# Optimization experiments

Measured on AMD Instinct MI355X. Metric: run time of the kernel, lower is better.

Reference implementation:

```python
import jax, jax.numpy as jnp
import numpy as np


def _conv(x, w, b, pad):
    y = jax.lax.conv_general_dilated(x, w, (1, 1), pad,
                                     dimension_numbers=('NCHW', 'OIHW', 'NCHW'))
    return y + b[None, :, None, None]


def _prelu(x, a):
    return jnp.where(x >= 0, x, a[None, :, None, None] * x)


def _pool2(x):
    # adaptive_avg_pool2d to exactly half resolution == 2x2 mean pooling
    B, C, H, W = x.shape
    return x.reshape(B, C, H // 2, 2, W // 2, 2).mean(axis=(3, 5))


def _l2norm(v, axis=-1):
    return v / jnp.maximum(jnp.linalg.norm(v, axis=axis, keepdims=True), 1e-12)


def _caun(x_low, ctx, w1, b1, a1, w2, b2, a2, kw, kb, sf=2):
    B, C, H, W = x_low.shape
    if ctx.shape[-2:] != (H, W):
        ctx = _pool2(ctx)
    f = _prelu(_conv(ctx, w1, b1, 'SAME'), a1)
    f = _prelu(_conv(f, w2, b2, 'SAME'), a2)
    mask = _conv(f, kw, kb, 'VALID')  # 1x1 conv -> [B, C*9*sf*sf, H, W]
    m = jax.nn.softmax(mask.reshape(B, C, 9, sf, sf, H, W), axis=2)
    xp = jnp.pad(x_low, ((0, 0), (0, 0), (1, 1), (1, 1)), mode='edge')
    # 3x3 neighborhoods in F.unfold row-major order -> [B, C, 9, H, W]
    neigh = jnp.stack([xp[:, :, i:i + H, j:j + W]
                       for i in range(3) for j in range(3)], axis=2)
    out = jnp.einsum('bcnuvhw,bcnhw->bcuvhw', m, neigh)  # [B,C,sf,sf,H,W]
    # faithful to torch permute(0,1,5,3,4,2).reshape(B,C,H*sf,W*sf)
    out = jnp.transpose(out, (0, 1, 5, 3, 4, 2)).reshape(B, C, H * sf, W * sf)
    return out


def _block(x, w1, b1, w2, b2):
    x = jax.nn.relu(_conv(x, w1, b1, 'SAME'))
    return jax.nn.relu(_conv(x, w2, b2, 'SAME'))


def setup_inputs() -> dict:
    key = jax.random.key(0)
    ks = iter(jax.random.split(key, 64))
    def rnd(shape, s=0.05):
        return jax.random.normal(next(ks), shape, jnp.float32) * s
    d = {}
    # encoder features (B=2, base 256x256, channels [32,64,128,256])
    d['x0_0'] = rnd((2, 32, 256, 256), 1.0)
    d['x1_0'] = rnd((2, 64, 128, 128), 1.0)
    d['x2_0'] = rnd((2, 128, 64, 64), 1.0)
    d['x3_0'] = rnd((2, 256, 32, 32), 1.0)
    # caun3: in=256, ctx=128
    d['c3_w1'] = rnd((128, 128, 3, 3)); d['c3_b1'] = jnp.zeros(128)
    d['c3_a1'] = 0.25 * jnp.ones(128)
    d['c3_w2'] = rnd((64, 128, 3, 3)); d['c3_b2'] = jnp.zeros(64)
    d['c3_a2'] = 0.25 * jnp.ones(64)
    d['c3_kw'] = rnd((256 * 36, 64, 1, 1)); d['c3_kb'] = jnp.zeros(256 * 36)
    # caun2: in=128, ctx=64
    d['c2_w1'] = rnd((64, 64, 3, 3)); d['c2_b1'] = jnp.zeros(64)
    d['c2_a1'] = 0.25 * jnp.ones(64)
    d['c2_w2'] = rnd((32, 64, 3, 3)); d['c2_b2'] = jnp.zeros(32)
    d['c2_a2'] = 0.25 * jnp.ones(32)
    d['c2_kw'] = rnd((128 * 36, 32, 1, 1)); d['c2_kb'] = jnp.zeros(128 * 36)
    # caun1: in=64, ctx=32
    d['c1_w1'] = rnd((32, 32, 3, 3)); d['c1_b1'] = jnp.zeros(32)
    d['c1_a1'] = 0.25 * jnp.ones(32)
    d['c1_w2'] = rnd((16, 32, 3, 3)); d['c1_b2'] = jnp.zeros(16)
    d['c1_a2'] = 0.25 * jnp.ones(16)
    d['c1_kw'] = rnd((64 * 36, 16, 1, 1)); d['c1_kb'] = jnp.zeros(64 * 36)
    # VGG-style conv blocks (conv3x3-ReLU x2)
    d['b21_w1'] = rnd((128, 384, 3, 3)); d['b21_b1'] = jnp.zeros(128)
    d['b21_w2'] = rnd((128, 128, 3, 3)); d['b21_b2'] = jnp.zeros(128)
    d['b12_w1'] = rnd((64, 192, 3, 3)); d['b12_b1'] = jnp.zeros(64)
    d['b12_w2'] = rnd((64, 64, 3, 3)); d['b12_b2'] = jnp.zeros(64)
    d['b03_w1'] = rnd((32, 96, 3, 3)); d['b03_b1'] = jnp.zeros(32)
    d['b03_w2'] = rnd((32, 32, 3, 3)); d['b03_b2'] = jnp.zeros(32)
    # final 1x1 conv -> num_classes=2
    d['fin_w'] = rnd((2, 32, 1, 1)); d['fin_b'] = jnp.zeros(2)
    # memory bank: 64 slots x 32 dims, row-normalized buffer
    d['mem'] = _l2norm(rnd((64, 32), 1.0))
    return d


def reference(x0_0, x1_0, x2_0, x3_0,
              c3_w1, c3_b1, c3_a1, c3_w2, c3_b2, c3_a2, c3_kw, c3_kb,
              c2_w1, c2_b1, c2_a1, c2_w2, c2_b2, c2_a2, c2_kw, c2_kb,
              c1_w1, c1_b1, c1_a1, c1_w2, c1_b2, c1_a2, c1_kw, c1_kb,
              b21_w1, b21_b1, b21_w2, b21_b2,
              b12_w1, b12_b1, b12_w2, b12_b2,
              b03_w1, b03_b1, b03_w2, b03_b2,
              fin_w, fin_b, mem):
    x3_up = _caun(x3_0, x2_0, c3_w1, c3_b1, c3_a1, c3_w2, c3_b2, c3_a2, c3_kw, c3_kb)
    x2_1 = _block(jnp.concatenate([x2_0, x3_up], axis=1), b21_w1, b21_b1, b21_w2, b21_b2)
    x2_up = _caun(x2_1, x1_0, c2_w1, c2_b1, c2_a1, c2_w2, c2_b2, c2_a2, c2_kw, c2_kb)
    x1_2 = _block(jnp.concatenate([x1_0, x2_up], axis=1), b12_w1, b12_b1, b12_w2, b12_b2)
    x1_up = _caun(x1_2, x0_0, c1_w1, c1_b1, c1_a1, c1_w2, c1_b2, c1_a2, c1_kw, c1_kb)
    x0_3 = _block(jnp.concatenate([x0_0, x1_up], axis=1), b03_w1, b03_b1, b03_w2, b03_b2)
    # memory bank residual fusion (eval mode: update=False)
    B, C, H, W = x0_3.shape
    feat = jnp.transpose(x0_3, (0, 2, 3, 1)).reshape(-1, C)
    fn = _l2norm(feat)
    mn = _l2norm(mem)
    attn = jax.nn.softmax(fn @ mn.T, axis=1)          # [BHW, num_slots]
    recon = (attn @ mn).reshape(B, H, W, C)
    x0_3 = x0_3 + jnp.transpose(recon, (0, 3, 1, 2))
    return _conv(x0_3, fin_w, fin_b, 'VALID')          # [B, num_classes, H, W]
```

## Files before the change

kernel.cpp:

```cpp
#include <hip/hip_runtime.h>
#include <hip/hip_bf16.h>
#include <math.h>

typedef __hip_bfloat16 bf16;
typedef short short8 __attribute__((ext_vector_type(8)));
typedef float f32x4 __attribute__((ext_vector_type(4)));

static __device__ __forceinline__ float b2f(bf16 x) { return __bfloat162float(x); }
static __device__ __forceinline__ bf16  f2b(float x) { return __float2bfloat16(x); }
static __device__ __forceinline__ short f2bs(float x) { bf16 t = f2b(x); return *reinterpret_cast<short*>(&t); }

static __device__ __forceinline__ float ldin(const void* p, size_t i, bool isb) {
    return isb ? b2f(((const bf16*)p)[i]) : ((const float*)p)[i];
}

__global__ void detect_kernel(const unsigned int* __restrict__ x, float* __restrict__ flagp) {
    __shared__ int sh[64];
    int insane = 0;
    for (int i = threadIdx.x; i < 1024; i += 64) {
        unsigned int lo = (x[i] & 0xFFFFu) << 16;
        float v = __uint_as_float(lo);
        if (!(fabsf(v) <= 1e6f)) insane++;
    }
    sh[threadIdx.x] = insane;
    __syncthreads();
    if (threadIdx.x == 0) {
        int t = 0;
        for (int i = 0; i < 64; ++i) t += sh[i];
        *flagp = (t < 16) ? 1.f : 0.f;
    }
}

__global__ void zfill(unsigned int* __restrict__ p, int nwords) {
    int i = blockIdx.x * blockDim.x + threadIdx.x;
    if (i < nwords) p[i] = 0u;
}

__global__ void diag_fill(unsigned int* __restrict__ out, int nwords, float val) {
    int i = blockIdx.x * blockDim.x + threadIdx.x;
    if (i < nwords) {
        unsigned short h = (unsigned short)(__float_as_uint(val) >> 16);
        out[i] = ((unsigned int)h << 16) | h;
    }
}

__global__ void wpack_kernel(const void* __restrict__ wt, const float* __restrict__ flg,
                             bf16* __restrict__ dst, int Cout, int Cin) {
    bool isb = (*flg != 0.f);
    int n = Cout * Cin * 9;
    int idx = blockIdx.x * blockDim.x + threadIdx.x;
    if (idx >= n) return;
    int ci = idx % Cin;
    int co = (idx / Cin) % Cout;
    int tap = idx / (Cin * Cout);
    dst[idx] = f2b(ldin(wt, ((size_t)co * Cin + ci) * 9 + tap, isb));
}

__global__ void b2bpack(const void* __restrict__ src, const float* __restrict__ flg,
                        bf16* __restrict__ dst, int n) {
    bool isb = (*flg != 0.f);
    int i = blockIdx.x * blockDim.x + threadIdx.x;
    if (i < n) dst[i] = f2b(ldin(src, i, isb));
}

__global__ void nchw2cl(const void* __restrict__ in, const float* __restrict__ flg,
                        bf16* __restrict__ out, int C, int HW) {
    __shared__ bf16 t[32][72];
    bool isb = (*flg != 0.f);
    int npx = HW >> 6, nc = C >> 5;
    int blk = blockIdx.x;
    int px0 = (blk % npx) << 6;
    int c0  = ((blk / npx) % nc) << 5;
    int b   = blk / (npx * nc);
    for (int i = threadIdx.x; i < 2048; i += 256) {
        int px = i & 63, c = i >> 6;
        t[c][px] = f2b(ldin(in, ((size_t)(b * C + c0 + c)) * HW + px0 + px, isb));
    }
    __syncthreads();
    for (int i = threadIdx.x; i < 2048; i += 256) {
        int c = i & 31, px = i >> 5;
        out[((size_t)b * HW + px0 + px) * C + c0 + c] = t[c][px];
    }
}

__global__ void pool2_cl(const void* __restrict__ in, const float* __restrict__ flg,
                         bf16* __restrict__ out, int B, int C, int H2, int W2) {
    bool isb = (*flg != 0.f);
    int idx = blockIdx.x * blockDim.x + threadIdx.x;
    int total = B * H2 * W2 * C;
    if (idx >= total) return;
    int c = idx % C;
    int pix = idx / C;
    int w = pix % W2;
    int h = (pix / W2) % H2;
    int b = pix / (W2 * H2);
    int H = H2 * 2, W = W2 * 2;
    size_t base = ((size_t)(b * C + c)) * H * W;
    float s = ldin(in, base + (size_t)(2*h)*W + 2*w, isb)   + ldin(in, base + (size_t)(2*h)*W + 2*w + 1, isb)
            + ldin(in, base + (size_t)(2*h+1)*W + 2*w, isb) + ldin(in, base + (size_t)(2*h+1)*W + 2*w + 1, isb);
    out[idx] = f2b(0.25f * s);
}

template<int RT>
__global__ __launch_bounds__(256) void conv3x3_lds(
        const bf16* __restrict__ in1, int C1,
        const bf16* __restrict__ in2, int C2,
        const bf16* __restrict__ wp,
        const void* __restrict__ bias,
        const void* __restrict__ alpha,
        const float* __restrict__ flg,
        const char* __restrict__ zs,
        bf16* __restrict__ out,
        int H, int W, int Cout, int act) {
    constexpr int NRB = 4 * RT + 2;
    constexpr int NIU = NRB * 18 * 4;
    constexpr int KI = (NIU + 255) / 256;
    constexpr int KW = 3;
    __shared__ bf16 in_s[2][NRB][18][36];
    __shared__ bf16 w_s[2][9][16][36];

    const bool isb = (*flg != 0.f);
    const int Cin = C1 + C2;
    const int tid = threadIdx.x;
    const int lane = tid & 63, wave = tid >> 6;
    const int quad = lane >> 4, l16 = lane & 15;
    const int cot = Cout >> 4;
    const int b = blockIdx.z / cot;
    const int co_base = (blockIdx.z % cot) << 4;
    const int r0b = blockIdx.y * (4 * RT);
    const int c0 = blockIdx.x << 4;
    const int cog = co_base + l16;

    const char* pin1[KI];
    const char* pin2[KI];
    #pragma unroll
    for (int k = 0; k < KI; ++k) {
        int u = min(tid + k * 256, NIU - 1);
        int sub = u & 3, px = (u >> 2) % 18, row = (u >> 2) / 18;
        int ih = r0b + row - 1, iw = c0 + px - 1;
        bool ok = (ih >= 0) && (ih < H) && (iw >= 0) && (iw < W);
        int ihc = min(max(ih, 0), H - 1), iwc = min(max(iw, 0), W - 1);
        size_t pix = (size_t)(b * H + ihc) * W + iwc;
        pin1[k] = (ok && C1 > 0) ? (const char*)(in1 + pix * C1 + sub * 8) : (zs + sub * 16);
        pin2[k] = ok ? (const char*)(in2 + pix * C2 + sub * 8) : (zs + sub * 16);
    }
    size_t offw[KW];
    #pragma unroll
    for (int k = 0; k < KW; ++k) {
        int u = min(tid + k * 256, 575);
        int sub = u & 3, cw = (u >> 2) & 15, tap = u >> 6;
        offw[k] = ((size_t)(tap * Cout + co_base + cw) * Cin + sub * 8) * 2;
    }
    const char* pw = (const char*)wp;

    short8 rin[KI], rwt[KW];
    auto issue = [&](int ci0) {
        const bool f1 = ci0 < C1;
        const int cl2 = (f1 ? ci0 : ci0 - C1) * 2;
        #pragma unroll
        for (int k = 0; k < KI; ++k)
            rin[k] = *(const short8*)((f1 ? pin1[k] : pin2[k]) + cl2);
        #pragma unroll
        for (int k = 0; k < KW; ++k)
            rwt[k] = *(const short8*)(pw + offw[k] + (size_t)ci0 * 2);
    };
    auto commit = [&](int bufi) {
        #pragma unroll
        for (int k = 0; k < KI; ++k) {
            int u = tid + k * 256;
            if (u < NIU) {
                int sub = u & 3, px = (u >> 2) % 18, row = (u >> 2) / 18;
                *(short8*)&in_s[bufi][row][px][sub * 8] = rin[k];
            }
        }
        #pragma unroll
        for (int k = 0; k < KW; ++k) {
            int u = tid + k * 256;
            if (u < 576) {
                int sub = u & 3, cw = (u >> 2) & 15, tap = u >> 6;
                *(short8*)&w_s[bufi][tap][cw][sub * 8] = rwt[k];
            }
        }
    };

    float bv = ldin(bias, cog, isb);
    f32x4 acc[RT];
    #pragma unroll
    for (int t = 0; t < RT; ++t) acc[t] = {bv, bv, bv, bv};

    const int nchunk = Cin >> 5;
    issue(0);
    commit(0);
    __syncthreads();
    int buf = 0;
    for (int ic = 0; ic < nchunk; ++ic) {
        const bool nx = (ic + 1 < nchunk);
        if (nx) issue((ic + 1) << 5);
        #pragma unroll
        for (int kw = 0; kw < 3; ++kw) {
            short8 F[RT + 2];
            #pragma unroll
            for (int j = 0; j < RT + 2; ++j)
                F[j] = *(const short8*)&in_s[buf][wave * RT + j][l16 + kw][quad * 8];
            #pragma unroll
            for (int kh = 0; kh < 3; ++kh) {
                short8 Wk = *(const short8*)&w_s[buf][kh * 3 + kw][l16][quad * 8];
                #pragma unroll
                for (int t = 0; t < RT; ++t)
                    acc[t] = __builtin_amdgcn_mfma_f32_16x16x32_bf16(F[t + kh], Wk, acc[t], 0, 0, 0);
            }
        }
        if (nx) commit(buf ^ 1);
        __syncthreads();
        buf ^= 1;
    }

    float a = (act == 2) ? ldin(alpha, cog, isb) : 0.f;
    const int r0 = r0b + wave * RT;
    #pragma unroll
    for (int t = 0; t < RT; ++t) {
        #pragma unroll
        for (int reg = 0; reg < 4; ++reg) {
            float v = acc[t][reg];
            if (act == 1) v = fmaxf(v, 0.f);
            else if (act == 2) v = (v >= 0.f) ? v : a * v;
            out[(((size_t)(b * H) + r0 + t) * W + c0 + (quad << 2) + reg) * Cout + cog] = f2b(v);
        }
    }
}

template<int RT>
__global__ __launch_bounds__(256) void conv3x3_ext(
        const void* __restrict__ in1, int C1,
        const bf16* __restrict__ in2, int C2,
        const bf16* __restrict__ wp,
        const void* __restrict__ bias,
        const void* __restrict__ alpha,
        const float* __restrict__ flg,
        bf16* __restrict__ out,
        int H, int W, int Cout, int act) {
    const bool isb = (*flg != 0.f);
    const int Cin = C1 + C2;
    const int lane = threadIdx.x & 63;
    const int wave = threadIdx.x >> 6;
    const int quad = lane >> 4, l16 = lane & 15;
    const int cot = Cout >> 4;
    const int b = blockIdx.z / cot;
    const int co_base = (blockIdx.z % cot) << 4;
    const int r0 = (blockIdx.y * 4 + wave) * RT;
    const int c0 = blockIdx.x << 4;
    const int cog = co_base + l16;

    float bv = ldin(bias, cog, isb);
    f32x4 acc[RT];
    #pragma unroll
    for (int t = 0; t < RT; ++t) acc[t] = {bv, bv, bv, bv};

    for (int ci0 = 0; ci0 < Cin; ci0 += 32) {
        const bool from1 = (ci0 < C1);
        #pragma unroll
        for (int kw = 0; kw < 3; ++kw) {
            const int iw = c0 + l16 + kw - 1;
            const bool okc = (iw >= 0) && (iw < W);
            short8 F[RT + 2];
            #pragma unroll
            for (int j = 0; j < RT + 2; ++j) {
                const int ih = r0 + j - 1;
                const bool ok = okc && (ih >= 0) && (ih < H);
                F[j] = short8{0, 0, 0, 0, 0, 0, 0, 0};
                if (from1) {
                    if (ok) {
                        size_t base = ((size_t)(b * C1 + ci0 + quad * 8)) * H * W
                                    + (size_t)ih * W + iw;
                        #pragma unroll
                        for (int jj = 0; jj < 8; ++jj)
                            F[j][jj] = f2bs(ldin(in1, base + (size_t)jj * H * W, isb));
                    }
                } else {
                    if (ok)
                        F[j] = *(const short8*)&in2[(((size_t)(b * H) + ih) * W + iw) * C2
                                                     + (ci0 - C1) + quad * 8];
                }
            }
            #pragma unroll
            for (int kh = 0; kh < 3; ++kh) {
                short8 bfrag = *(const short8*)&wp[((size_t)(kh * 3 + kw) * Cout + cog) * Cin
                                                   + ci0 + quad * 8];
                #pragma unroll
                for (int t = 0; t < RT; ++t)
                    acc[t] = __builtin_amdgcn_mfma_f32_16x16x32_bf16(F[t + kh], bfrag, acc[t], 0, 0, 0);
            }
        }
    }

    float a = (act == 2) ? ldin(alpha, cog, isb) : 0.f;
    #pragma unroll
    for (int t = 0; t < RT; ++t) {
        #pragma unroll
        for (int reg = 0; reg < 4; ++reg) {
            float v = acc[t][reg];
            if (act == 1) v = fmaxf(v, 0.f);
            else if (act == 2) v = (v >= 0.f) ? v : a * v;
            out[(((size_t)(b * H) + r0 + t) * W + c0 + (quad << 2) + reg) * Cout + cog] = f2b(v);
        }
    }
}

template<int CC>
__global__ __launch_bounds__(256) void caun_v4(
        const bf16* __restrict__ f,
        const void* __restrict__ xlow, int xext,
        const bf16* __restrict__ kwp,
        const void* __restrict__ kb,
        const float* __restrict__ flg,
        bf16* __restrict__ out,
        int C, int K, int H, int W) {
    __shared__ float kb_s[CC * 40];
    __shared__ bf16  neigh_s[100 * (CC + 2)];
    __shared__ bf16  out_s[256 * (CC + 2)];

    const bool isb = (*flg != 0.f);
    const int tw = W >> 3;
    const int h0 = (blockIdx.x / tw) << 3;
    const int w0 = (blockIdx.x % tw) << 3;
    const int b  = blockIdx.y;
    const int c0 = blockIdx.z * CC;
    const int tid = threadIdx.x, wave = tid >> 6, lane = tid & 63;
    const int quad = lane >> 4, l16 = lane & 15;

    for (int i = tid; i < 100 * CC; i += 256) {
        int c = i % CC, cell = i / CC;
        int r = cell / 10, q = cell % 10;
        int ih = min(max(h0 + r - 1, 0), H - 1);
        int iw = min(max(w0 + q - 1, 0), W - 1);
        float v = xext
            ? ldin(xlow, ((size_t)(b * C + c0 + c)) * H * W + (size_t)ih * W + iw, isb)
            : b2f(((const bf16*)xlow)[(((size_t)(b * H) + ih) * W + iw) * C + c0 + c]);
        neigh_s[cell * (CC + 2) + c] = f2b(v);
    }
    for (int i = tid; i < 36 * CC; i += 256) {
        int j = i % 36, c = i / 36;
        kb_s[c * 40 + j] = ldin(kb, (size_t)(c0 + c) * 36 + j, isb);
    }

    const int hl = (wave << 1) + (l16 >> 3);
    const int wl = l16 & 7;
    const size_t fpx = ((size_t)b * H * W + (size_t)(h0 + hl) * W + (w0 + wl)) * K;
    const int nkc = ((K + 31) & ~31) >> 5;
    const short8 z8 = {0, 0, 0, 0, 0, 0, 0, 0};
    short8 Bf[2];
    {
        int kq0 = quad * 8;
        Bf[0] = (kq0 < K) ? *(const short8*)&f[fpx + kq0] : z8;
        Bf[1] = (nkc > 1) ? *(const short8*)&f[fpx + 32 + quad * 8] : z8;
    }
    __syncthreads();

    const int nA = quad, nB = 4 + quad;
    const bf16* nbA = neigh_s + ((hl + nA / 3) * 10 + wl + nA % 3) * (CC + 2);
    const bf16* nbB = neigh_s + ((hl + nB / 3) * 10 + wl + nB % 3) * (CC + 2);
    const bf16* nbC = neigh_s + ((hl + 2) * 10 + wl + 2) * (CC + 2);
    const int xaddr = ((lane ^ 32) & 63) << 2;
    const bool q0 = (quad == 0);
    bf16* osl = out_s + ((wave << 6) + lane) * (CC + 2);

    for (int c = 0; c < CC; ++c) {
        const size_t crow = (size_t)(c0 + c) * 36;
        const float* kbc = kb_s + c * 40;
        f32x4 a0 = *(const f32x4*)(kbc + (quad << 2));
        f32x4 a1 = *(const f32x4*)(kbc + 16 + (quad << 2));
        f32x4 a2 = *(const f32x4*)(kbc + 32);
        #pragma unroll
        for (int ch = 0; ch < 2; ++ch) {
            if (ch >= nkc) break;
            int kq = ch * 32 + quad * 8;
            bool kok = kq < K;
            short8 f0 = kok ? *(const short8*)&kwp[(crow + l16) * K + kq] : z8;
            short8 f1 = kok ? *(const short8*)&kwp[(crow + 16 + l16) * K + kq] : z8;
            short8 f2 = (kok && l16 < 4) ? *(const short8*)&kwp[(crow + 32 + l16) * K + kq] : z8;
            a0 = __builtin_amdgcn_mfma_f32_16x16x32_bf16(f0, Bf[ch], a0, 0, 0, 0);
            a1 = __builtin_amdgcn_mfma_f32_16x16x32_bf16(f1, Bf[ch], a1, 0, 0, 0);
            a2 = __builtin_amdgcn_mfma_f32_16x16x32_bf16(f2, Bf[ch], a2, 0, 0, 0);
        }
        float nv0 = b2f(nbA[c]), nv1 = b2f(nbB[c]), nv8 = b2f(nbC[c]);
        float S[4], A[4];
        #pragma unroll
        for (int r = 0; r < 4; ++r) {
            float e0 = __expf(a0[r]);
            float e1 = __expf(a1[r]);
            float e2 = q0 ? __expf(a2[r]) : 0.f;
            float sp = e0 + e1 + e2;
            float ap = fmaf(e2, nv8, fmaf(e1, nv1, e0 * nv0));
            sp += __int_as_float(__builtin_amdgcn_ds_swizzle(__float_as_int(sp), 0x401F));
            ap += __int_as_float(__builtin_amdgcn_ds_swizzle(__float_as_int(ap), 0x401F));
            sp += __int_as_float(__builtin_amdgcn_ds_bpermute(xaddr, __float_as_int(sp)));
            ap += __int_as_float(__builtin_amdgcn_ds_bpermute(xaddr, __float_as_int(ap)));
            S[r] = sp; A[r] = ap;
        }
        float se = (quad == 0) ? S[0] : (quad == 1) ? S[1] : (quad == 2) ? S[2] : S[3];
        float av = (quad == 0) ? A[0] : (quad == 1) ? A[1] : (quad == 2) ? A[2] : A[3];
        osl[c] = f2b(__fdividef(av, se));
    }

    __syncthreads();
    const size_t obase = (size_t)b * 4 * H * W;
    for (int i = tid; i < 256 * CC; i += 256) {
        int c = i % CC, s = i / CC;
        int wv = s >> 6, q = (s >> 4) & 3, hb = (s >> 3) & 1, wls = s & 7;
        int row_l = (wls << 1) + (q & 1);
        int col_l = (((wv << 1) + hb) << 1) + (q >> 1);
        size_t P = obase + (size_t)(2 * w0 + row_l) * (2 * W) + (2 * h0 + col_l);
        out[P * C + c0 + c] = out_s[s * (CC + 2) + c];
    }
}

__global__ void memnorm_kernel(const void* __restrict__ mem, const float* __restrict__ flg,
                               float* __restrict__ mn) {
    bool isb = (*flg != 0.f);
    int s = threadIdx.x;
    float v[32];
    float ss = 0.f;
    #pragma unroll
    for (int c = 0; c < 32; ++c) { v[c] = ldin(mem, s * 32 + c, isb); ss += v[c] * v[c]; }
    float inv = 1.f / fmaxf(sqrtf(ss), 1e-12f);
    #pragma unroll
    for (int c = 0; c < 32; ++c) mn[s * 32 + c] = v[c] * inv;
}

__global__ __launch_bounds__(256, 2) void memfuse_kernel(
        bf16* __restrict__ x, const float* __restrict__ mn) {
    __shared__ float mns[64 * 32];
    for (int i = threadIdx.x; i < 64 * 32; i += blockDim.x) mns[i] = mn[i];
    __syncthreads();
    int idx = blockIdx.x * blockDim.x + threadIdx.x;
    bf16* xp = x + (size_t)idx * 32;

    float feat[32];
    float ss = 0.f;
    #pragma unroll
    for (int c = 0; c < 32; ++c) { feat[c] = b2f(xp[c]); ss += feat[c] * feat[c]; }
    float inv = 1.f / fmaxf(sqrtf(ss), 1e-12f);

    float se = 0.f;
    float racc[32];
    #pragma unroll
    for (int c = 0; c < 32; ++c) racc[c] = 0.f;

    for (int s = 0; s < 64; ++s) {
        const float* mr = mns + s * 32;
        float dot = 0.f;
        #pragma unroll
        for (int c = 0; c < 32; ++c) dot = fmaf(feat[c], mr[c], dot);
        float e = __expf(dot * inv);
        se += e;
        #pragma unroll
        for (int c = 0; c < 32; ++c) racc[c] = fmaf(e, mr[c], racc[c]);
    }
    float rse = 1.f / se;
    #pragma unroll
    for (int c = 0; c < 32; ++c)
        xp[c] = f2b(feat[c] + racc[c] * rse);
}

__global__ void final1x1_kernel(const bf16* __restrict__ x,
                                const void* __restrict__ fw, const void* __restrict__ fb,
                                const float* __restrict__ flg,
                                void* __restrict__ out, int HW) {
    bool isb = (*flg != 0.f);
    int idx = blockIdx.x * blockDim.x + threadIdx.x;
    int b = idx / HW, p = idx % HW;
    const bf16* xp = x + (size_t)idx * 32;
    float a0 = ldin(fb, 0, isb), a1 = ldin(fb, 1, isb);
    #pragma unroll
    for (int c = 0; c < 32; ++c) {
        float v = b2f(xp[c]);
        a0 = fmaf(v, ldin(fw, c, isb), a0);
        a1 = fmaf(v, ldin(fw, 32 + c, isb), a1);
    }
    size_t i0 = (size_t)b * 2 * HW + p;
    size_t i1 = i0 + HW;
    if (isb) { ((bf16*)out)[i0] = f2b(a0); ((bf16*)out)[i1] = f2b(a1); }
    else     { ((float*)out)[i0] = a0;     ((float*)out)[i1] = a1; }
}

extern "C" void kernel_launch(void* const* d_in, const int* in_sizes, int n_in,
                              void* d_out, int out_size, void* d_ws, size_t ws_size,
                              hipStream_t stream) {
    const void* x0_0 = d_in[0];
    const void* x1_0 = d_in[1];
    const void* x2_0 = d_in[2];
    const void* x3_0 = d_in[3];
    const void* c3_w1 = d_in[4];  const void* c3_b1 = d_in[5];  const void* c3_a1 = d_in[6];
    const void* c3_w2 = d_in[7];  const void* c3_b2 = d_in[8];  const void* c3_a2 = d_in[9];
    const void* c3_kw = d_in[10]; const void* c3_kb = d_in[11];
    const void* c2_w1 = d_in[12]; const void* c2_b1 = d_in[13]; const void* c2_a1 = d_in[14];
    const void* c2_w2 = d_in[15]; const void* c2_b2 = d_in[16]; const void* c2_a2 = d_in[17];
    const void* c2_kw = d_in[18]; const void* c2_kb = d_in[19];
    const void* c1_w1 = d_in[20]; const void* c1_b1 = d_in[21]; const void* c1_a1 = d_in[22];
    const void* c1_w2 = d_in[23]; const void* c1_b2 = d_in[24]; const void* c1_a2 = d_in[25];
    const void* c1_kw = d_in[26]; const void* c1_kb = d_in[27];
    const void* b21_w1 = d_in[28]; const void* b21_b1 = d_in[29];
    const void* b21_w2 = d_in[30]; const void* b21_b2 = d_in[31];
    const void* b12_w1 = d_in[32]; const void* b12_b1 = d_in[33];
    const void* b12_w2 = d_in[34]; const void* b12_b2 = d_in[35];
    const void* b03_w1 = d_in[36]; const void* b03_b1 = d_in[37];
    const void* b03_w2 = d_in[38]; const void* b03_b2 = d_in[39];
    const void* fin_w = d_in[40];  const void* fin_b = d_in[41];
    const void* memw  = d_in[42];
    (void)in_sizes; (void)n_in;

    const int TB = 256;
    auto blocks = [](int n) { return (n + 255) / 256; };

    const size_t NEED = 25165824 + 65536;
    if (ws_size < NEED) {
        diag_fill<<<blocks(out_size / 2), TB, 0, stream>>>(
            (unsigned int*)d_out, out_size / 2, (float)ws_size);
        return;
    }
    const size_t NEED_X0 = 25165824 + 8388608 + 65536 + 256;
    const bool have_x0cl = (ws_size >= NEED_X0);

    size_t tail = (ws_size - 65536) & ~(size_t)255;
    bf16*  wtail = (bf16*)((char*)d_ws + tail);
    float* mn    = (float*)((char*)d_ws + tail + 55296);
    float* flg   = (float*)((char*)d_ws + tail + 63488);
    char*  zstrip = (char*)d_ws + tail + 63744;

    bf16* A = (bf16*)d_ws;
    bf16* x3up  = A + 0;
    bf16* ctx3p = A + 2097152;
    bf16* f3a   = A + 2359296;
    bf16* f3b   = A + 2621440;
    bf16* kw3p  = A + 3000000;
    bf16* t2a   = A + 2097152;
    bf16* x2cl  = A + 3145728;
    bf16* x2_1  = A + 0;
    bf16* ctx2  = A + 1048576;
    bf16* f2a   = A + 1572864;
    bf16* f2b   = A + 2097152;
    bf16* x2up  = A + 2359296;
    bf16* t1a   = A + 0;
    bf16* x1cl  = A + 6995968;
    bf16* x1_2  = A + 10485760;
    bf16* ctx1  = A + 4194304;
    bf16* f1a   = A + 5242880;
    bf16* f1b   = A + 9437184;
    bf16* kw1p  = A + 8388608;
    bf16* x1up  = A + 0;
    bf16* t0a   = A + 8388608;
    bf16* x0_3  = A + 0;
    bf16* wslot = A + 6553600;
    bf16* x0cl  = A + 12582912;

    detect_kernel<<<1, 64, 0, stream>>>((const unsigned int*)x0_0, flg);
    zfill<<<1, TB, 0, stream>>>((unsigned int*)zstrip, 256);

    auto wpk = [&](const void* w, bf16* dst, int Cout, int Cin) {
        wpack_kernel<<<blocks(Cout * Cin * 9), TB, 0, stream>>>(w, flg, dst, Cout, Cin);
    };
    auto cg2 = [](int H, int W, int Cout) {
        return dim3(W >> 4, H >> 3, 2 * (Cout >> 4));
    };

    if (have_x0cl)
        nchw2cl<<<2 * 1 * 1024, TB, 0, stream>>>(x0_0, flg, x0cl, 32, 65536);

    pool2_cl<<<blocks(262144), TB, 0, stream>>>(x2_0, flg, ctx3p, 2, 128, 32, 32);
    wpk(c3_w1, wslot, 128, 128);
    conv3x3_lds<2><<<cg2(32, 32, 128), TB, 0, stream>>>(
        nullptr, 0, ctx3p, 128, wslot, c3_b1, c3_a1, flg, zstrip, f3a, 32, 32, 128, 2);
    wpk(c3_w2, wslot, 64, 128);
    conv3x3_lds<2><<<cg2(32, 32, 64), TB, 0, stream>>>(
        nullptr, 0, f3a, 128, wslot, c3_b2, c3_a2, flg, zstrip, f3b, 32, 32, 64, 2);
    b2bpack<<<blocks(256 * 36 * 64), TB, 0, stream>>>(c3_kw, flg, kw3p, 256 * 36 * 64);
    caun_v4<16><<<dim3(16, 2, 16), TB, 0, stream>>>(
        f3b, x3_0, 1, kw3p, c3_kb, flg, x3up, 256, 64, 32, 32);

    nchw2cl<<<2 * 4 * 64, TB, 0, stream>>>(x2_0, flg, x2cl, 128, 4096);
    wpk(b21_w1, wslot, 128, 384);
    conv3x3_lds<2><<<cg2(64, 64, 128), TB, 0, stream>>>(
        x2cl, 128, x3up, 256, wslot, b21_b1, nullptr, flg, zstrip, t2a, 64, 64, 128, 1);
    wpk(b21_w2, wslot, 128, 128);
    conv3x3_lds<2><<<cg2(64, 64, 128), TB, 0, stream>>>(
        nullptr, 0, t2a, 128, wslot, b21_b2, nullptr, flg, zstrip, x2_1, 64, 64, 128, 1);

    pool2_cl<<<blocks(524288), TB, 0, stream>>>(x1_0, flg, ctx2, 2, 64, 64, 64);
    wpk(c2_w1, wslot, 64, 64);
    conv3x3_lds<2><<<cg2(64, 64, 64), TB, 0, stream>>>(
        nullptr, 0, ctx2, 64, wslot, c2_b1, c2_a1, flg, zstrip, f2a, 64, 64, 64, 2);
    wpk(c2_w2, wslot, 32, 64);
    conv3x3_lds<2><<<cg2(64, 64, 32), TB, 0, stream>>>(
        nullptr, 0, f2a, 64, wslot, c2_b2, c2_a2, flg, zstrip, f2b, 64, 64, 32, 2);
    b2bpack<<<blocks(128 * 36 * 32), TB, 0, stream>>>(c2_kw, flg, wslot, 128 * 36 * 32);
    caun_v4<16><<<dim3(64, 2, 8), TB, 0, stream>>>(
        f2b, x2_1, 0, wslot, c2_kb, flg, x2up, 128, 32, 64, 64);

    nchw2cl<<<2 * 2 * 256, TB, 0, stream>>>(x1_0, flg, x1cl, 64, 16384);
    wpk(b12_w1, wslot, 64, 192);
    conv3x3_lds<2><<<cg2(128, 128, 64), TB, 0, stream>>>(
        x1cl, 64, x2up, 128, wslot, b12_b1, nullptr, flg, zstrip, t1a, 128, 128, 64, 1);
    wpk(b12_w2, wslot, 64, 64);
    conv3x3_lds<2><<<cg2(128, 128, 64), TB, 0, stream>>>(
        nullptr, 0, t1a, 64, wslot, b12_b2, nullptr, flg, zstrip, x1_2, 128, 128, 64, 1);

    pool2_cl<<<blocks(1048576), TB, 0, stream>>>(x0_0, flg, ctx1, 2, 32, 128, 128);
    wpk(c1_w1, wslot, 32, 32);
    conv3x3_lds<2><<<cg2(128, 128, 32), TB, 0, stream>>>(
        nullptr, 0, ctx1, 32, wslot, c1_b1, c1_a1, flg, zstrip, f1a, 128, 128, 32, 2);
    wpk(c1_w2, wslot, 16, 32);
    conv3x3_lds<2><<<cg2(128, 128, 16), TB, 0, stream>>>(
        nullptr, 0, f1a, 32, wslot, c1_b2, c1_a2, flg, zstrip, f1b, 128, 128, 16, 2);
    b2bpack<<<blocks(64 * 36 * 16), TB, 0, stream>>>(c1_kw, flg, kw1p, 64 * 36 * 16);
    caun_v4<16><<<dim3(256, 2, 4), TB, 0, stream>>>(
        f1b, x1_2, 0, kw1p, c1_kb, flg, x1up, 64, 16, 128, 128);

    wpk(b03_w1, wtail, 32, 96);
    if (have_x0cl) {
        conv3x3_lds<2><<<cg2(256, 256, 32), TB, 0, stream>>>(
            x0cl, 32, x1up, 64, wtail, b03_b1, nullptr, flg, zstrip, t0a, 256, 256, 32, 1);
    } else {
        conv3x3_ext<4><<<dim3(16, 16, 4), TB, 0, stream>>>(
            x0_0, 32, x1up, 64, wtail, b03_b1, nullptr, flg, t0a, 256, 256, 32, 1);
    }
    wpk(b03_w2, wtail, 32, 32);
    conv3x3_lds<2><<<cg2(256, 256, 32), TB, 0, stream>>>(
        nullptr, 0, t0a, 32, wtail, b03_b2, nullptr, flg, zstrip, x0_3, 256, 256, 32, 1);

    memnorm_kernel<<<1, 64, 0, stream>>>(memw, flg, mn);
    memfuse_kernel<<<512, TB, 0, stream>>>(x0_3, mn);
    final1x1_kernel<<<512, TB, 0, stream>>>(x0_3, fin_w, fin_b, flg, d_out, 256 * 256);
}
```

Measured before the change: 471.8 us.

## Fuse memory-bank norm, residual fusion and final 1x1 conv; streamline CAUN softmax reduction

Merges the memory-normalisation, memory-fusion and final 1x1 conv kernels into one kernel. Each block renormalises the 64x32 memory bank in shared memory, and the residual result feeds the 1x1 conv directly, so x0_3 is never written back and re-read and two launches go away. The memfuse exponent now uses a raw v_exp_f32 with a pre-scaled log2e factor. The CAUN kernel uses pointer-increment weight addressing, a 2x unrolled channel loop, and a transpose-style cross-lane reduction that needs 4 bpermutes plus 2 swizzles instead of 8 of each per channel. Memory normalisation is now repeated redundantly in every block.

```diff
diff --git a/kernel.cpp b/kernel.cpp
--- a/kernel.cpp
+++ b/kernel.cpp
@@ -9,6 +9,7 @@
 static __device__ __forceinline__ float b2f(bf16 x) { return __bfloat162float(x); }
 static __device__ __forceinline__ bf16  f2b(float x) { return __float2bfloat16(x); }
 static __device__ __forceinline__ short f2bs(float x) { bf16 t = f2b(x); return *reinterpret_cast<short*>(&t); }
+static __device__ __forceinline__ float ex2(float x) { float r; asm("v_exp_f32 %0, %1" : "=v"(r) : "v"(x)); return r; }
 
 static __device__ __forceinline__ float ldin(const void* p, size_t i, bool isb) {
     return isb ? b2f(((const bf16*)p)[i]) : ((const float*)p)[i];
@@ -307,7 +308,7 @@
 }
 
 template<int CC>
-__global__ __launch_bounds__(256) void caun_v4(
+__global__ __launch_bounds__(256) void caun_v5(
         const bf16* __restrict__ f,
         const void* __restrict__ xlow, int xext,
         const bf16* __restrict__ kwp,
@@ -360,12 +361,20 @@
     const bf16* nbA = neigh_s + ((hl + nA / 3) * 10 + wl + nA % 3) * (CC + 2);
     const bf16* nbB = neigh_s + ((hl + nB / 3) * 10 + wl + nB % 3) * (CC + 2);
     const bf16* nbC = neigh_s + ((hl + 2) * 10 + wl + 2) * (CC + 2);
-    const int xaddr = ((lane ^ 32) & 63) << 2;
+    const int x32 = ((lane ^ 32) & 63) << 2;
     const bool q0 = (quad == 0);
+    const bool bhi = (quad >> 1) != 0;
+    const bool blo = (quad & 1) != 0;
+    const bool l4 = (l16 < 4);
     bf16* osl = out_s + ((wave << 6) + lane) * (CC + 2);
 
+    const char* pk = (const char*)kwp + (((size_t)c0 * 36 + l16) * K + quad * 8) * 2;
+    const int dkc = 36 * K * 2;
+    const int d16 = 16 * K * 2;
+    const int d32 = 32 * K * 2;
+
+    #pragma unroll 2
     for (int c = 0; c < CC; ++c) {
-        const size_t crow = (size_t)(c0 + c) * 36;
         const float* kbc = kb_s + c * 40;
         f32x4 a0 = *(const f32x4*)(kbc + (quad << 2));
         f32x4 a1 = *(const f32x4*)(kbc + 16 + (quad << 2));
@@ -373,33 +382,45 @@
         #pragma unroll
         for (int ch = 0; ch < 2; ++ch) {
             if (ch >= nkc) break;
-            int kq = ch * 32 + quad * 8;
-            bool kok = kq < K;
-            short8 f0 = kok ? *(const short8*)&kwp[(crow + l16) * K + kq] : z8;
-            short8 f1 = kok ? *(const short8*)&kwp[(crow + 16 + l16) * K + kq] : z8;
-            short8 f2 = (kok && l16 < 4) ? *(const short8*)&kwp[(crow + 32 + l16) * K + kq] : z8;
+            bool kok = (ch * 32 + quad * 8) < K;
+            short8 f0 = kok ? *(const short8*)(pk + ch * 64) : z8;
+            short8 f1 = kok ? *(const short8*)(pk + d16 + ch * 64) : z8;
+            short8 f2 = (kok && l4) ? *(const short8*)(pk + d32 + ch * 64) : z8;
             a0 = __builtin_amdgcn_mfma_f32_16x16x32_bf16(f0, Bf[ch], a0, 0, 0, 0);
             a1 = __builtin_amdgcn_mfma_f32_16x16x32_bf16(f1, Bf[ch], a1, 0, 0, 0);
             a2 = __builtin_amdgcn_mfma_f32_16x16x32_bf16(f2, Bf[ch], a2, 0, 0, 0);
         }
+        pk += dkc;
         float nv0 = b2f(nbA[c]), nv1 = b2f(nbB[c]), nv8 = b2f(nbC[c]);
-        float S[4], A[4];
+        float Vs[4], Va[4];
         #pragma unroll
         for (int r = 0; r < 4; ++r) {
             float e0 = __expf(a0[r]);
             float e1 = __expf(a1[r]);
-            float e2 = q0 ? __expf(a2[r]) : 0.f;
-            float sp = e0 + e1 + e2;
-            float ap = fmaf(e2, nv8, fmaf(e1, nv1, e0 * nv0));
-            sp += __int_as_float(__builtin_amdgcn_ds_swizzle(__float_as_int(sp), 0x401F));
-            ap += __int_as_float(__builtin_amdgcn_ds_swizzle(__float_as_int(ap), 0x401F));
-            sp += __int_as_float(__builtin_amdgcn_ds_bpermute(xaddr, __float_as_int(sp)));
-            ap += __int_as_float(__builtin_amdgcn_ds_bpermute(xaddr, __float_as_int(ap)));
-            S[r] = sp; A[r] = ap;
-        }
-        float se = (quad == 0) ? S[0] : (quad == 1) ? S[1] : (quad == 2) ? S[2] : S[3];
-        float av = (quad == 0) ? A[0] : (quad == 1) ? A[1] : (quad == 2) ? A[2] : A[3];
-        osl[c] = f2b(__fdividef(av, se));
+            float e2 = __expf(a2[r]);
+            float e2m = q0 ? e2 : 0.f;
+            Vs[r] = e0 + e1 + e2m;
+            Va[r] = fmaf(e0, nv0, fmaf(e1, nv1, e2m * nv8));
+        }
+        float sd0 = bhi ? Vs[0] : Vs[2];
+        float sd1 = bhi ? Vs[1] : Vs[3];
+        float sa0 = bhi ? Va[0] : Va[2];
+        float sa1 = bhi ? Va[1] : Va[3];
+        float rs0 = __int_as_float(__builtin_amdgcn_ds_bpermute(x32, __float_as_int(sd0)));
+        float rs1 = __int_as_float(__builtin_amdgcn_ds_bpermute(x32, __float_as_int(sd1)));
+        float ra0 = __int_as_float(__builtin_amdgcn_ds_bpermute(x32, __float_as_int(sa0)));
+        float ra1 = __int_as_float(__builtin_amdgcn_ds_bpermute(x32, __float_as_int(sa1)));
+        float Ps0 = (bhi ? Vs[2] : Vs[0]) + rs0;
+        float Ps1 = (bhi ? Vs[3] : Vs[1]) + rs1;
+        float Pa0 = (bhi ? Va[2] : Va[0]) + ra0;
+        float Pa1 = (bhi ? Va[3] : Va[1]) + ra1;
+        float ss = blo ? Ps0 : Ps1;
+        float sa = blo ? Pa0 : Pa1;
+        float qs = __int_as_float(__builtin_amdgcn_ds_swizzle(__float_as_int(ss), 0x401F));
+        float qa = __int_as_float(__builtin_amdgcn_ds_swizzle(__float_as_int(sa), 0x401F));
+        float Ss = (blo ? Ps1 : Ps0) + qs;
+        float Sa = (blo ? Pa1 : Pa0) + qa;
+        osl[c] = f2b(__fdividef(Sa, Ss));
     }
 
     __syncthreads();
@@ -414,32 +435,39 @@
     }
 }
 
-__global__ void memnorm_kernel(const void* __restrict__ mem, const float* __restrict__ flg,
-                               float* __restrict__ mn) {
-    bool isb = (*flg != 0.f);
-    int s = threadIdx.x;
-    float v[32];
-    float ss = 0.f;
-    #pragma unroll
-    for (int c = 0; c < 32; ++c) { v[c] = ldin(mem, s * 32 + c, isb); ss += v[c] * v[c]; }
-    float inv = 1.f / fmaxf(sqrtf(ss), 1e-12f);
-    #pragma unroll
-    for (int c = 0; c < 32; ++c) mn[s * 32 + c] = v[c] * inv;
-}
-
-__global__ __launch_bounds__(256, 2) void memfuse_kernel(
-        bf16* __restrict__ x, const float* __restrict__ mn) {
+__global__ __launch_bounds__(256, 2) void memfuse_final(
+        const bf16* __restrict__ x, const void* __restrict__ memw,
+        const void* __restrict__ fw, const void* __restrict__ fb,
+        const float* __restrict__ flg, void* __restrict__ out, int HW) {
     __shared__ float mns[64 * 32];
-    for (int i = threadIdx.x; i < 64 * 32; i += blockDim.x) mns[i] = mn[i];
+    __shared__ float fws[66];
+    const bool isb = (*flg != 0.f);
+    if (threadIdx.x < 64) {
+        int s = threadIdx.x;
+        float v[32];
+        float ss = 0.f;
+        #pragma unroll
+        for (int c = 0; c < 32; ++c) { v[c] = ldin(memw, s * 32 + c, isb); ss += v[c] * v[c]; }
+        float inv = 1.f / fmaxf(sqrtf(ss), 1e-12f);
+        #pragma unroll
+        for (int c = 0; c < 32; ++c) mns[s * 32 + c] = v[c] * inv;
+    } else if (threadIdx.x < 128) {
+        int t = threadIdx.x - 64;
+        fws[t] = ldin(fw, t, isb);
+    } else if (threadIdx.x == 128) {
+        fws[64] = ldin(fb, 0, isb);
+        fws[65] = ldin(fb, 1, isb);
+    }
     __syncthreads();
+
     int idx = blockIdx.x * blockDim.x + threadIdx.x;
-    bf16* xp = x + (size_t)idx * 32;
+    const bf16* xp = x + (size_t)idx * 32;
 
     float feat[32];
     float ss = 0.f;
     #pragma unroll
     for (int c = 0; c < 32; ++c) { feat[c] = b2f(xp[c]); ss += feat[c] * feat[c]; }
-    float inv = 1.f / fmaxf(sqrtf(ss), 1e-12f);
+    float inv2 = 1.4426950408889634f / fmaxf(sqrtf(ss), 1e-12f);
 
     float se = 0.f;
     float racc[32];
@@ -451,32 +479,20 @@
         float dot = 0.f;
         #pragma unroll
         for (int c = 0; c < 32; ++c) dot = fmaf(feat[c], mr[c], dot);
-        float e = __expf(dot * inv);
+        float e = ex2(dot * inv2);
         se += e;
         #pragma unroll
         for (int c = 0; c < 32; ++c) racc[c] = fmaf(e, mr[c], racc[c]);
     }
     float rse = 1.f / se;
-    #pragma unroll
-    for (int c = 0; c < 32; ++c)
-        xp[c] = f2b(feat[c] + racc[c] * rse);
-}
-
-__global__ void final1x1_kernel(const bf16* __restrict__ x,
-                                const void* __restrict__ fw, const void* __restrict__ fb,
-                                const float* __restrict__ flg,
-                                void* __restrict__ out, int HW) {
-    bool isb = (*flg != 0.f);
-    int idx = blockIdx.x * blockDim.x + threadIdx.x;
+    float a0 = fws[64], a1 = fws[65];
+    #pragma unroll
+    for (int c = 0; c < 32; ++c) {
+        float y = feat[c] + racc[c] * rse;
+        a0 = fmaf(y, fws[c], a0);
+        a1 = fmaf(y, fws[32 + c], a1);
+    }
     int b = idx / HW, p = idx % HW;
-    const bf16* xp = x + (size_t)idx * 32;
-    float a0 = ldin(fb, 0, isb), a1 = ldin(fb, 1, isb);
-    #pragma unroll
-    for (int c = 0; c < 32; ++c) {
-        float v = b2f(xp[c]);
-        a0 = fmaf(v, ldin(fw, c, isb), a0);
-        a1 = fmaf(v, ldin(fw, 32 + c, isb), a1);
-    }
     size_t i0 = (size_t)b * 2 * HW + p;
     size_t i1 = i0 + HW;
     if (isb) { ((bf16*)out)[i0] = f2b(a0); ((bf16*)out)[i1] = f2b(a1); }
@@ -523,7 +539,6 @@
 
     size_t tail = (ws_size - 65536) & ~(size_t)255;
     bf16*  wtail = (bf16*)((char*)d_ws + tail);
-    float* mn    = (float*)((char*)d_ws + tail + 55296);
     float* flg   = (float*)((char*)d_ws + tail + 63488);
     char*  zstrip = (char*)d_ws + tail + 63744;
 
@@ -574,7 +589,7 @@
     conv3x3_lds<2><<<cg2(32, 32, 64), TB, 0, stream>>>(
         nullptr, 0, f3a, 128, wslot, c3_b2, c3_a2, flg, zstrip, f3b, 32, 32, 64, 2);
     b2bpack<<<blocks(256 * 36 * 64), TB, 0, stream>>>(c3_kw, flg, kw3p, 256 * 36 * 64);
-    caun_v4<16><<<dim3(16, 2, 16), TB, 0, stream>>>(
+    caun_v5<16><<<dim3(16, 2, 16), TB, 0, stream>>>(
         f3b, x3_0, 1, kw3p, c3_kb, flg, x3up, 256, 64, 32, 32);
 
     nchw2cl<<<2 * 4 * 64, TB, 0, stream>>>(x2_0, flg, x2cl, 128, 4096);
@@ -593,7 +608,7 @@
     conv3x3_lds<2><<<cg2(64, 64, 32), TB, 0, stream>>>(
         nullptr, 0, f2a, 64, wslot, c2_b2, c2_a2, flg, zstrip, f2b, 64, 64, 32, 2);
     b2bpack<<<blocks(128 * 36 * 32), TB, 0, stream>>>(c2_kw, flg, wslot, 128 * 36 * 32);
-    caun_v4<16><<<dim3(64, 2, 8), TB, 0, stream>>>(
+    caun_v5<16><<<dim3(64, 2, 8), TB, 0, stream>>>(
         f2b, x2_1, 0, wslot, c2_kb, flg, x2up, 128, 32, 64, 64);
 
     nchw2cl<<<2 * 2 * 256, TB, 0, stream>>>(x1_0, flg, x1cl, 64, 16384);
@@ -612,7 +627,7 @@
     conv3x3_lds<2><<<cg2(128, 128, 16), TB, 0, stream>>>(
         nullptr, 0, f1a, 32, wslot, c1_b2, c1_a2, flg, zstrip, f1b, 128, 128, 16, 2);
     b2bpack<<<blocks(64 * 36 * 16), TB, 0, stream>>>(c1_kw, flg, kw1p, 64 * 36 * 16);
-    caun_v4<16><<<dim3(256, 2, 4), TB, 0, stream>>>(
+    caun_v5<16><<<dim3(256, 2, 4), TB, 0, stream>>>(
         f1b, x1_2, 0, kw1p, c1_kb, flg, x1up, 64, 16, 128, 128);
 
     wpk(b03_w1, wtail, 32, 96);
@@ -627,7 +642,5 @@
     conv3x3_lds<2><<<cg2(256, 256, 32), TB, 0, stream>>>(
         nullptr, 0, t0a, 32, wtail, b03_b2, nullptr, flg, zstrip, x0_3, 256, 256, 32, 1);
 
-    memnorm_kernel<<<1, 64, 0, stream>>>(memw, flg, mn);
-    memfuse_kernel<<<512, TB, 0, stream>>>(x0_3, mn);
-    final1x1_kernel<<<512, TB, 0, stream>>>(x0_3, fin_w, fin_b, flg, d_out, 256 * 256);
-}
+    memfuse_final<<<512, TB, 0, stream>>>(x0_3, memw, fin_w, fin_b, flg, d_out, 256 * 256);
+}
```

Result: faster. 458.7 us (-2.8%).
